# Kernel optimization log

Hardware: AMD Instinct MI355X
Metric: run time of the kernel (lower is better)

Reference implementation:

```python
import jax, jax.numpy as jnp
import numpy as np

H = 1024
IN = 512
B = 32
E_H = 0.5
Z_MIN = 0.001
Z_MAX = 0.1
DT = 1.0


def setup_inputs() -> dict:
    key = jax.random.key(0)
    ks = jax.random.split(key, 10)
    s = 1.0 / np.sqrt(H)
    uni = lambda k, shape: jax.random.uniform(k, shape, jnp.float32, -s, s)
    return {
        "x": jax.random.normal(ks[0], (IN, B), jnp.float32),
        "h": jax.random.uniform(ks[1], (B, H), jnp.float32),      # hidden state [B,H]
        "X": jnp.ones((B, H, H), jnp.float32),                     # resources
        "U": jnp.full((B, H, H), 0.9, jnp.float32),                # utilization (init 0.9)
        "c_x": uni(ks[2], (H, H)),
        "c_u": uni(ks[3], (H, H)),
        "c_U": uni(ks[4], (H, H)),
        "c_h": uni(ks[5], (H, 1)),
        "w": uni(ks[6], (H, H)),
        "p": uni(ks[7], (H, IN)),
        "b": uni(ks[8], (H, 1)),
    }


def reference(x, h, X, U, c_x, c_u, c_U, c_h, w, p, b):
    sig = jax.nn.sigmoid
    hb = h[:, :, None]                                  # h[b,j] broadcast over k -> [B,H,1]
    # resource (X) update: z_x + (1-z_x)*X - dt*U*X*h
    z_x = Z_MIN + (Z_MAX - Z_MIN) * sig(c_x)            # [H,H]
    X_new = z_x + (1.0 - z_x) * X - DT * U * (X * hb)   # [B,H,H]
    # utilization (U) update, clamped to [Ucap (detached), 1]
    z_u = Z_MIN + (Z_MAX - Z_MIN) * sig(c_u)            # [H,H]
    Ucap = 0.9 * sig(c_U)                               # [H,H]
    U_new = Ucap * z_u + (1.0 - z_u) * U + DT * Ucap * ((1.0 - U) * hb)
    U_new = jnp.clip(U_new, jax.lax.stop_gradient(Ucap), 1.0)
    # hidden update with dynamic weights W = w * U * X (per batch)
    z_h = E_H * sig(c_h)                                # [H,1]
    W = w * U_new * X_new                               # [B,H,H]
    rec = jnp.einsum("bjk,bk->jb", W, h)               # [H,B]
    pre = rec + p @ x + b                               # [H,B]
    h_newT = (1.0 - z_h) * h.T + z_h * sig(pre)         # [H,B]
    return h_newT.T                                     # [B,H]
```

## Files before the change

kernel.cpp:

```cpp
#include <hip/hip_runtime.h>

#define HH 1024
#define INW 512
#define BB 32
#define Z_MIN_C 0.001f
#define Z_RANGE_C 0.099f
#define E_H_C 0.5f

typedef float v4f __attribute__((ext_vector_type(4)));

__device__ __forceinline__ float sigmoidf_(float v) {
    return 1.0f / (1.0f + __expf(-v));
}

__global__ __launch_bounds__(256) void param_kernel(
    const float* __restrict__ c_x,
    const float* __restrict__ c_u,
    const float* __restrict__ c_U,
    float* __restrict__ zxA, float* __restrict__ ozuA,
    float* __restrict__ ucA, float* __restrict__ AA)
{
    const int idx = blockIdx.x * HH + threadIdx.x * 4;
    v4f cx4 = __builtin_nontemporal_load((const v4f*)(c_x + idx));
    v4f cu4 = __builtin_nontemporal_load((const v4f*)(c_u + idx));
    v4f cC4 = __builtin_nontemporal_load((const v4f*)(c_U + idx));
    v4f zx4, ozu4, uc4, A4;
    #pragma unroll
    for (int c = 0; c < 4; ++c) {
        float zx = Z_MIN_C + Z_RANGE_C * sigmoidf_(cx4[c]);
        float zu = Z_MIN_C + Z_RANGE_C * sigmoidf_(cu4[c]);
        float uc = 0.9f * sigmoidf_(cC4[c]);
        zx4[c] = zx;
        ozu4[c] = 1.0f - zu;
        uc4[c] = uc;
        A4[c] = uc * zu;
    }
    *(v4f*)(zxA + idx) = zx4;
    *(v4f*)(ozuA + idx) = ozu4;
    *(v4f*)(ucA + idx) = uc4;
    *(v4f*)(AA + idx) = A4;
}

__global__ __launch_bounds__(256) void px_kernel(
    const float* __restrict__ x,
    const float* __restrict__ p,
    const float* __restrict__ bias,
    float* __restrict__ pre0)
{
    const int wv = threadIdx.x >> 6;
    const int lane = threadIdx.x & 63;
    const int j = blockIdx.x * 4 + wv;
    const int b = lane & 31;
    const int half = lane >> 5;

    const float* pr = p + j * INW + half * 256;
    const float* xc = x + (half * 256) * BB + b;
    float acc = 0.0f;
    #pragma unroll 8
    for (int i = 0; i < 256; ++i)
        acc = fmaf(pr[i], xc[i * BB], acc);
    acc += __shfl_xor(acc, 32);
    if (lane < 32)
        pre0[lane * HH + j] = acc + bias[j];
}

__global__ __launch_bounds__(256, 4) void stp_fused(
    const float* __restrict__ h,
    const float* __restrict__ X,
    const float* __restrict__ U,
    const float* __restrict__ c_h,
    const float* __restrict__ w,
    const float* __restrict__ zxA,
    const float* __restrict__ ozuA,
    const float* __restrict__ ucA,
    const float* __restrict__ AA,
    const float* __restrict__ pre0,
    float* __restrict__ out)
{
    const int bid = blockIdx.x;
    const int j = bid & (HH - 1);
    const int b = bid >> 10;
    const int t = threadIdx.x;
    const int lane = t & 63;
    const int wave = t >> 6;
    const int k0 = t * 4;

    __shared__ float rec_part[4];

    const int rowbase = bid * HH;
    v4f Xv = __builtin_nontemporal_load((const v4f*)(X + rowbase + k0));
    v4f Uv = __builtin_nontemporal_load((const v4f*)(U + rowbase + k0));
    v4f hk = *(const v4f*)(h + b * HH + k0);
    const float hjv = h[bid];
    const float pv = pre0[bid];
    const float chj = c_h[j];

    const int pbase = j * HH + k0;
    v4f zx4 = *(const v4f*)(zxA + pbase);
    v4f ozu4 = *(const v4f*)(ozuA + pbase);
    v4f uc4 = *(const v4f*)(ucA + pbase);
    v4f A4 = *(const v4f*)(AA + pbase);
    v4f wv4 = *(const v4f*)(w + pbase);

    float ss = 0.0f;
    #pragma unroll
    for (int c = 0; c < 4; ++c) {
        const float uh = uc4[c] * hjv;
        float Un = fmaf(ozu4[c] - uh, Uv[c], A4[c] + uh);
        Un = fminf(fmaxf(Un, uc4[c]), 1.0f);
        float Xn = fmaf(1.0f - zx4[c], Xv[c], zx4[c]);
        Xn = fmaf(-Uv[c], Xv[c] * hjv, Xn);
        ss = fmaf(wv4[c] * hk[c], Un * Xn, ss);
    }

    #pragma unroll
    for (int off = 32; off > 0; off >>= 1)
        ss += __shfl_xor(ss, off);
    if (lane == 0) rec_part[wave] = ss;
    __syncthreads();

    if (t == 0) {
        const float rec = rec_part[0] + rec_part[1] + rec_part[2] + rec_part[3];
        const float pre = pv + rec;
        const float zh = E_H_C * sigmoidf_(chj);
        out[bid] = (1.0f - zh) * hjv + zh * sigmoidf_(pre);
    }
}

extern "C" void kernel_launch(void* const* d_in, const int* in_sizes, int n_in,
                              void* d_out, int out_size, void* d_ws, size_t ws_size,
                              hipStream_t stream) {
    const float* x   = (const float*)d_in[0];
    const float* h   = (const float*)d_in[1];
    const float* X   = (const float*)d_in[2];
    const float* U   = (const float*)d_in[3];
    const float* c_x = (const float*)d_in[4];
    const float* c_u = (const float*)d_in[5];
    const float* c_U = (const float*)d_in[6];
    const float* c_h = (const float*)d_in[7];
    const float* w   = (const float*)d_in[8];
    const float* p   = (const float*)d_in[9];
    const float* b   = (const float*)d_in[10];
    float* out = (float*)d_out;

    float* ws = (float*)d_ws;
    float* pre0 = ws;
    float* zxA  = ws + 32768;
    float* ozuA = zxA + HH * HH;
    float* ucA  = ozuA + HH * HH;
    float* AA   = ucA + HH * HH;

    param_kernel<<<HH, 256, 0, stream>>>(c_x, c_u, c_U, zxA, ozuA, ucA, AA);
    px_kernel<<<HH / 4, 256, 0, stream>>>(x, p, b, pre0);
    stp_fused<<<BB * HH, 256, 0, stream>>>(h, X, U, c_h, w, zxA, ozuA, ucA, AA,
                                           pre0, out);
}
```

Baseline: 329.0 us.

## Process eight batches per block to reuse per-row parameters and prefetch X/U

Each block of the main kernel now handles one row j across 8 batch entries instead of one, so the per-(j,k) parameter vectors (zx, 1-zu, Ucap, A, w) are loaded once and reused eight times. X/U/h rows are double-buffered with a 4-deep register ring to keep loads in flight. Grid shrinks from 32768 to 4096 blocks. This trades higher register use, and possibly lower occupancy, for less parameter traffic and fewer block launches.

```diff
diff --git a/kernel.cpp b/kernel.cpp
--- a/kernel.cpp
+++ b/kernel.cpp
@@ -3,6 +3,7 @@
 #define HH 1024
 #define INW 512
 #define BB 32
+#define BG 8
 #define Z_MIN_C 0.001f
 #define Z_RANGE_C 0.099f
 #define E_H_C 0.5f
@@ -77,23 +78,25 @@
     const float* __restrict__ pre0,
     float* __restrict__ out)
 {
-    const int bid = blockIdx.x;
-    const int j = bid & (HH - 1);
-    const int b = bid >> 10;
+    const int j = blockIdx.x & (HH - 1);
+    const int g = blockIdx.x >> 10;
+    const int b0 = g * BG;
     const int t = threadIdx.x;
     const int lane = t & 63;
     const int wave = t >> 6;
     const int k0 = t * 4;
 
-    __shared__ float rec_part[4];
+    __shared__ float rec_part[BG][4];
 
-    const int rowbase = bid * HH;
-    v4f Xv = __builtin_nontemporal_load((const v4f*)(X + rowbase + k0));
-    v4f Uv = __builtin_nontemporal_load((const v4f*)(U + rowbase + k0));
-    v4f hk = *(const v4f*)(h + b * HH + k0);
-    const float hjv = h[bid];
-    const float pv = pre0[bid];
-    const float chj = c_h[j];
+    v4f Xs[4], Us[4], hs[4];
+    #pragma unroll
+    for (int i = 0; i < 4; ++i) {
+        const int b = b0 + i;
+        const int rb = (b * HH + j) * HH + k0;
+        Xs[i] = __builtin_nontemporal_load((const v4f*)(X + rb));
+        Us[i] = __builtin_nontemporal_load((const v4f*)(U + rb));
+        hs[i] = *(const v4f*)(h + b * HH + k0);
+    }
 
     const int pbase = j * HH + k0;
     v4f zx4 = *(const v4f*)(zxA + pbase);
@@ -102,28 +105,55 @@
     v4f A4 = *(const v4f*)(AA + pbase);
     v4f wv4 = *(const v4f*)(w + pbase);
 
-    float ss = 0.0f;
+    float hj[BG];
     #pragma unroll
-    for (int c = 0; c < 4; ++c) {
-        const float uh = uc4[c] * hjv;
-        float Un = fmaf(ozu4[c] - uh, Uv[c], A4[c] + uh);
-        Un = fminf(fmaxf(Un, uc4[c]), 1.0f);
-        float Xn = fmaf(1.0f - zx4[c], Xv[c], zx4[c]);
-        Xn = fmaf(-Uv[c], Xv[c] * hjv, Xn);
-        ss = fmaf(wv4[c] * hk[c], Un * Xn, ss);
+    for (int i = 0; i < BG; ++i) hj[i] = h[(b0 + i) * HH + j];
+
+    float s[BG];
+    #pragma unroll
+    for (int i = 0; i < BG; ++i) {
+        const int sl = i & 3;
+        v4f Xv = Xs[sl];
+        v4f Uv = Us[sl];
+        v4f hk = hs[sl];
+        if (i + 4 < BG) {
+            const int b = b0 + i + 4;
+            const int rb = (b * HH + j) * HH + k0;
+            Xs[sl] = __builtin_nontemporal_load((const v4f*)(X + rb));
+            Us[sl] = __builtin_nontemporal_load((const v4f*)(U + rb));
+            hs[sl] = *(const v4f*)(h + b * HH + k0);
+        }
+        const float hjv = hj[i];
+        float ss = 0.0f;
+        #pragma unroll
+        for (int c = 0; c < 4; ++c) {
+            const float uh = uc4[c] * hjv;
+            float Un = fmaf(ozu4[c] - uh, Uv[c], A4[c] + uh);
+            Un = fminf(fmaxf(Un, uc4[c]), 1.0f);
+            float Xn = fmaf(1.0f - zx4[c], Xv[c], zx4[c]);
+            Xn = fmaf(-Uv[c], Xv[c] * hjv, Xn);
+            ss = fmaf(wv4[c] * hk[c], Un * Xn, ss);
+        }
+        s[i] = ss;
     }
 
     #pragma unroll
-    for (int off = 32; off > 0; off >>= 1)
-        ss += __shfl_xor(ss, off);
-    if (lane == 0) rec_part[wave] = ss;
+    for (int i = 0; i < BG; ++i) {
+        float v = s[i];
+        #pragma unroll
+        for (int off = 32; off > 0; off >>= 1)
+            v += __shfl_xor(v, off);
+        if (lane == 0) rec_part[i][wave] = v;
+    }
     __syncthreads();
 
-    if (t == 0) {
-        const float rec = rec_part[0] + rec_part[1] + rec_part[2] + rec_part[3];
-        const float pre = pv + rec;
-        const float zh = E_H_C * sigmoidf_(chj);
-        out[bid] = (1.0f - zh) * hjv + zh * sigmoidf_(pre);
+    if (t < BG) {
+        const int b = b0 + t;
+        const float rec = rec_part[t][0] + rec_part[t][1] + rec_part[t][2] + rec_part[t][3];
+        const float pre = pre0[b * HH + j] + rec;
+        const float zh = E_H_C * sigmoidf_(c_h[j]);
+        const float hv = h[b * HH + j];
+        out[b * HH + j] = (1.0f - zh) * hv + zh * sigmoidf_(pre);
     }
 }
 
@@ -152,6 +182,6 @@
 
     param_kernel<<<HH, 256, 0, stream>>>(c_x, c_u, c_U, zxA, ozuA, ucA, AA);
     px_kernel<<<HH / 4, 256, 0, stream>>>(x, p, b, pre0);
-    stp_fused<<<BB * HH, 256, 0, stream>>>(h, X, U, c_h, w, zxA, ozuA, ucA, AA,
-                                           pre0, out);
+    stp_fused<<<HH * 4, 256, 0, stream>>>(h, X, U, c_h, w, zxA, ozuA, ucA, AA,
+                                          pre0, out);
 }
```

Result: faster. 312.4 us (-5.1%).
